# Kernel optimization log

Hardware: AMD Instinct MI355X
Metric: run time of the kernel (lower is better)

The kernel has to match this reference:

```python
import jax, jax.numpy as jnp
import numpy as np

HEAD_SIZE = 128


def setup_inputs() -> dict:
    key = jax.random.key(0)
    ks = jax.random.split(key, 6)
    B, T, C, HS, HO = 8, 2048, 1024, 128, 128
    return {
        "q": jax.random.normal(ks[0], (B, T, C), dtype=jnp.float32),
        "k": jax.random.normal(ks[1], (B, T, C), dtype=jnp.float32),
        "v": jax.random.normal(ks[2], (B, T, C), dtype=jnp.float32),
        "Wq": jax.random.normal(ks[3], (C, HS), dtype=jnp.float32) * (C ** -0.5),
        "Wk": jax.random.normal(ks[4], (C, HS), dtype=jnp.float32) * (C ** -0.5),
        "Wv": jax.random.normal(ks[5], (C, HO), dtype=jnp.float32) * (C ** -0.5),
    }


def reference(q, k, v, Wq, Wk, Wv):
    # q,k,v: [B,T,C]; Wq,Wk: [C,HS]; Wv: [C,HO]
    T = q.shape[1]
    Q = jnp.einsum("btc,ch->bth", q, Wq)  # [B,T,HS]
    K = jnp.einsum("btc,ch->bth", k, Wk)  # [B,T,HS]
    V = jnp.einsum("btc,co->bto", v, Wv)  # [B,T,HO]
    scores = jnp.einsum("bqh,bkh->bqk", Q, K)  # [B,T,T]
    # tril(ones, diagonal=1): allowed where j <= i+1; mask (set -inf) where j > i+1
    i = jnp.arange(T)[:, None]
    j = jnp.arange(T)[None, :]
    allowed = j <= i + 1  # faithful to diagonal=1 quirk
    scores = jnp.where(allowed, scores, -jnp.inf)
    weights = jax.nn.softmax(scores * (HEAD_SIZE ** -0.5), axis=-1)
    return jnp.einsum("bqk,bko->bqo", weights, V)  # [B,T,HO]
```

## Files before the change

kernel.cpp:

```cpp
#include <hip/hip_runtime.h>

typedef short short8 __attribute__((ext_vector_type(8)));
typedef float f32x4 __attribute__((ext_vector_type(4)));
typedef unsigned short ushort_t;

__device__ inline ushort_t f2bf(float f) {
    union { float f; unsigned int u; } x{f};
    unsigned int r = (x.u + 0x7fffu + ((x.u >> 16) & 1u)) >> 16;
    return (ushort_t)r;
}
__device__ inline float bf2f(ushort_t u) {
    union { unsigned int u; float f; } x{(unsigned int)u << 16};
    return x.f;
}

__device__ inline void gload_lds16(const void* g, void* l) {
    __builtin_amdgcn_global_load_lds(
        (const __attribute__((address_space(1))) unsigned int*)g,
        (__attribute__((address_space(3))) unsigned int*)l, 16, 0, 0);
}

template <int CTRL>
__device__ inline float dppadd(float x) {
    union { float f; int i; } u, v;
    u.f = x;
    v.i = __builtin_amdgcn_update_dpp(0, u.i, CTRL, 0xf, 0xf, true);
    return x + v.f;
}
#define DPP_XOR1 0xB1
#define DPP_XOR2 0x4E
#define DPP_HMIR 0x141
#define DPP_MIR  0x140

__global__ __launch_bounds__(1024) void wt_prep(const float* __restrict__ Wq,
                                                const float* __restrict__ Wk,
                                                const float* __restrict__ Wv,
                                                ushort_t* __restrict__ Wt) {
    __shared__ float t[32][33];
    int bz = blockIdx.z;
    const float* W = bz == 0 ? Wq : (bz == 1 ? Wk : Wv);
    int h0 = blockIdx.x * 32, c0 = blockIdx.y * 32;
    int tx = threadIdx.x, ty = threadIdx.y;
    t[ty][tx] = W[(c0 + ty) * 128 + h0 + tx];
    __syncthreads();
    Wt[bz * 131072 + (h0 + ty) * 1024 + c0 + tx] = f2bf(t[tx][ty]);
}

__global__ __launch_bounds__(256, 4) void proj_gemm(const float* __restrict__ q,
                                                    const float* __restrict__ k,
                                                    const float* __restrict__ v,
                                                    const ushort_t* __restrict__ Wt,
                                                    ushort_t* __restrict__ Qb,
                                                    ushort_t* __restrict__ Kb,
                                                    ushort_t* __restrict__ Vt) {
    __shared__ ushort_t lA[64][72];
    __shared__ ushort_t lB[128][72];
    int z = blockIdx.z;
    const float* X = z == 0 ? q : (z == 1 ? k : v);
    const ushort_t* Wz = Wt + z * 131072;
    int m0 = blockIdx.x * 64;
    int tid = threadIdx.x;
    int lane = tid & 63, wv = tid >> 6;
    int g = lane >> 4, li = lane & 15;

    f32x4 z4 = {0.f, 0.f, 0.f, 0.f};
    f32x4 acc[8];
#pragma unroll
    for (int n = 0; n < 8; ++n) acc[n] = z4;

    for (int ks = 0; ks < 16; ++ks) {
        int k0 = ks * 64;
        if (ks) __syncthreads();
#pragma unroll
        for (int it = 0; it < 4; ++it) {
            int idx = it * 256 + tid;
            int row = idx >> 4, c4 = idx & 15;
            const float4 val = *(const float4*)(X + (size_t)(m0 + row) * 1024 + k0 + c4 * 4);
            ushort4 bb;
            bb.x = f2bf(val.x); bb.y = f2bf(val.y); bb.z = f2bf(val.z); bb.w = f2bf(val.w);
            *(ushort4*)&lA[row][c4 * 4] = bb;
        }
#pragma unroll
        for (int it = 0; it < 4; ++it) {
            int idx = it * 256 + tid;
            int h = idx >> 3, k8 = idx & 7;
            *(int4*)&lB[h][k8 * 8] = *(const int4*)(Wz + h * 1024 + k0 + k8 * 8);
        }
        __syncthreads();
#pragma unroll
        for (int kk = 0; kk < 2; ++kk) {
            short8 a = *(const short8*)&lA[wv * 16 + li][kk * 32 + g * 8];
            short8 b[8];
#pragma unroll
            for (int n = 0; n < 8; ++n)
                b[n] = *(const short8*)&lB[n * 16 + li][kk * 32 + g * 8];
#pragma unroll
            for (int n = 0; n < 8; ++n)
                acc[n] = __builtin_amdgcn_mfma_f32_16x16x32_bf16(a, b[n], acc[n], 0, 0, 0);
        }
    }
    if (z < 2) {
        ushort_t* Out = z == 0 ? Qb : Kb;
        int rbase = m0 + wv * 16 + g * 4;
#pragma unroll
        for (int n = 0; n < 8; ++n)
#pragma unroll
            for (int r = 0; r < 4; ++r)
                Out[(size_t)(rbase + r) * 128 + n * 16 + li] = f2bf(acc[n][r]);
    } else {
        int tbase = m0 + wv * 16 + g * 4;
#pragma unroll
        for (int n = 0; n < 8; ++n)
#pragma unroll
            for (int r = 0; r < 4; ++r) {
                int t = tbase + r;
                int bb = t >> 11, tl = t & 2047;
                Vt[((size_t)bb * 128 + n * 16 + li) * 2048 + tl] = f2bf(acc[n][r]);
            }
    }
}

__global__ __launch_bounds__(256) void attn_fwd(const ushort_t* __restrict__ Qb,
                                                const ushort_t* __restrict__ Kb,
                                                const ushort_t* __restrict__ Vt,
                                                ushort_t* __restrict__ oPb,
                                                float* __restrict__ lPf) {
    constexpr float SCL = 0.08838834764831845f * 1.4426950408889634f;
    constexpr float MB  = 8.0f * 1.4426950408889634f;
    __shared__ ushort_t Kl[2][64][128];
    __shared__ ushort_t Vl[2][128][64];
    __shared__ ushort_t lP[4][16][72];

    int t = threadIdx.x;
    int lane = t & 63, wv = t >> 6;
    int g = lane >> 4, li = lane & 15;
    int b = blockIdx.x & 7;
    int idx = blockIdx.x >> 3;
    int qb = 31 - (idx >> 1);
    int s  = idx & 1;
    int r0 = qb * 64 + wv * 16;
    int NT = qb + 2; if (NT > 32) NT = 32;
    int h0 = (NT + 1) >> 1;
    int jb = s ? h0 : 0;
    int je = s ? NT : h0;
    const ushort_t* kb0 = Kb + (size_t)b * 2048 * 128;
    const ushort_t* vb0 = Vt + (size_t)b * 128 * 2048;
    ushort_t (*P)[72] = lP[wv];

    short8 qf[4];
    const ushort_t* qrow = Qb + (size_t)(b * 2048 + r0 + li) * 128 + g * 8;
#pragma unroll
    for (int kf = 0; kf < 4; ++kf) qf[kf] = *(const short8*)(qrow + kf * 32);

    f32x4 z4 = {0.f, 0.f, 0.f, 0.f};
    f32x4 o[8];
#pragma unroll
    for (int n = 0; n < 8; ++n) o[n] = z4;
    float lr[4] = {0.f, 0.f, 0.f, 0.f};

    auto STAGE = [&](int jt, int buf) {
        int j0 = jt * 64;
#pragma unroll
        for (int r = 0; r < 4; ++r) {
            int row = r * 16 + (t >> 4);
            int c = (t & 15) ^ ((t >> 4) & 7);
            gload_lds16(kb0 + (size_t)(j0 + row) * 128 + c * 8,
                        (char*)&Kl[buf][0][0] + r * 4096 + t * 16);
        }
#pragma unroll
        for (int r = 0; r < 4; ++r) {
            int row = r * 32 + (t >> 3);
            int c = (t & 7) ^ ((t >> 3) & 7);
            gload_lds16(vb0 + (size_t)row * 2048 + j0 + c * 8,
                        (char*)&Vl[buf][0][0] + r * 4096 + t * 16);
        }
    };

    STAGE(jb, 0);
    asm volatile("s_waitcnt vmcnt(0)" ::: "memory");
    __builtin_amdgcn_s_barrier();

    for (int jt = jb; jt < je; ++jt) {
        int buf = (jt - jb) & 1;
        int j0 = jt * 64;
        if (jt + 1 < je) STAGE(jt + 1, buf ^ 1);
        const char* kb = (const char*)&Kl[buf][0][0];
        const char* vb = (const char*)&Vl[buf][0][0];

        f32x4 sA[4];
#pragma unroll
        for (int jf = 0; jf < 4; ++jf) sA[jf] = z4;
#pragma unroll
        for (int jf = 0; jf < 4; ++jf)
#pragma unroll
            for (int kf = 0; kf < 4; ++kf) {
                short8 kfrag = *(const short8*)(kb + (jf * 16 + li) * 256 +
                                                (((kf * 4 + g) ^ (li & 7)) * 16));
                sA[jf] = __builtin_amdgcn_mfma_f32_16x16x32_bf16(qf[kf], kfrag, sA[jf], 0, 0, 0);
            }
        if (j0 + 63 > r0 + 1) {
#pragma unroll
            for (int jf = 0; jf < 4; ++jf)
#pragma unroll
                for (int r = 0; r < 4; ++r) {
                    int j = j0 + jf * 16 + li;
                    int i = r0 + g * 4 + r;
                    if (j > i + 1) sA[jf][r] = -1e30f;
                }
        }
#pragma unroll
        for (int jf = 0; jf < 4; ++jf)
#pragma unroll
            for (int r = 0; r < 4; ++r) {
                float p = exp2f(sA[jf][r] * SCL - MB);
                lr[r] += p;
                P[g * 4 + r][jf * 16 + li] = f2bf(p);
            }
        asm volatile("s_waitcnt lgkmcnt(0)" ::: "memory");
        __builtin_amdgcn_sched_barrier(0);
        short8 pa0 = *(const short8*)&P[li][g * 8];
        short8 pa1 = *(const short8*)&P[li][32 + g * 8];
#pragma unroll
        for (int n = 0; n < 8; ++n) {
            short8 vf = *(const short8*)(vb + (n * 16 + li) * 128 +
                                         ((g ^ (li & 7)) * 16));
            o[n] = __builtin_amdgcn_mfma_f32_16x16x32_bf16(pa0, vf, o[n], 0, 0, 0);
        }
#pragma unroll
        for (int n = 0; n < 8; ++n) {
            short8 vf = *(const short8*)(vb + (n * 16 + li) * 128 +
                                         (((4 + g) ^ (li & 7)) * 16));
            o[n] = __builtin_amdgcn_mfma_f32_16x16x32_bf16(pa1, vf, o[n], 0, 0, 0);
        }
        asm volatile("s_waitcnt vmcnt(0)" ::: "memory");
        __builtin_amdgcn_s_barrier();
    }

#pragma unroll
    for (int r = 0; r < 4; ++r) {
        lr[r] = dppadd<DPP_XOR1>(lr[r]);
        lr[r] = dppadd<DPP_XOR2>(lr[r]);
        lr[r] = dppadd<DPP_HMIR>(lr[r]);
        lr[r] = dppadd<DPP_MIR>(lr[r]);
    }
    if (li == 0) {
#pragma unroll
        for (int r = 0; r < 4; ++r)
            lPf[s * 16384 + b * 2048 + r0 + g * 4 + r] = lr[r];
    }
#pragma unroll
    for (int r = 0; r < 4; ++r) {
        size_t base = ((size_t)s * 16384 + b * 2048 + r0 + g * 4 + r) * 128 + li;
#pragma unroll
        for (int n = 0; n < 8; ++n)
            oPb[base + n * 16] = f2bf(o[n][r]);
    }
}

__global__ __launch_bounds__(256) void attn_combine(const ushort_t* __restrict__ oPb,
                                                    const float* __restrict__ lPf,
                                                    float* __restrict__ Out) {
    int gid = blockIdx.x * 256 + threadIdx.x;
    int row = gid >> 4;
    int c8 = (gid & 15) * 8;
    float inv = 1.0f / (lPf[row] + lPf[16384 + row]);
    const ushort_t* p0 = oPb + (size_t)row * 128 + c8;
    const ushort_t* p1 = p0 + (size_t)16384 * 128;
    short8 a = *(const short8*)p0;
    short8 bb = *(const short8*)p1;
    float* op = Out + (size_t)row * 128 + c8;
    float4 r0v, r1v;
    float* rp0 = (float*)&r0v;
    float* rp1 = (float*)&r1v;
#pragma unroll
    for (int j = 0; j < 4; ++j)
        rp0[j] = (bf2f((ushort_t)a[j]) + bf2f((ushort_t)bb[j])) * inv;
#pragma unroll
    for (int j = 0; j < 4; ++j)
        rp1[j] = (bf2f((ushort_t)a[4 + j]) + bf2f((ushort_t)bb[4 + j])) * inv;
    *(float4*)op = r0v;
    *(float4*)(op + 4) = r1v;
}

extern "C" void kernel_launch(void* const* d_in, const int* in_sizes, int n_in,
                              void* d_out, int out_size, void* d_ws, size_t ws_size,
                              hipStream_t stream) {
    const float* q  = (const float*)d_in[0];
    const float* k  = (const float*)d_in[1];
    const float* v  = (const float*)d_in[2];
    const float* Wq = (const float*)d_in[3];
    const float* Wk = (const float*)d_in[4];
    const float* Wv = (const float*)d_in[5];
    float* Out = (float*)d_out;

    ushort_t* Qb  = (ushort_t*)d_ws;
    ushort_t* Kb  = Qb + 2097152;
    ushort_t* Vt  = Kb + 2097152;
    ushort_t* Wt  = Vt + 2097152;
    ushort_t* oPb = Wt + 393216;
    float*    lPf = (float*)(oPb + 4194304);

    wt_prep<<<dim3(4, 32, 3), dim3(32, 32), 0, stream>>>(Wq, Wk, Wv, Wt);
    proj_gemm<<<dim3(256, 1, 3), 256, 0, stream>>>(q, k, v, Wt, Qb, Kb, Vt);
    attn_fwd<<<dim3(512), 256, 0, stream>>>(Qb, Kb, Vt, oPb, lPf);
    attn_combine<<<dim3(1024), 256, 0, stream>>>(oPb, lPf, Out);
}
```

Measured before the change: 79.26 us.

## Keep softmax probabilities in registers by transposing the QK^T MFMA

The QK^T MFMA operands are swapped so each lane holds scores for one query row across several keys. Those values can then be packed straight into the A-operand fragments of the PV MFMA. This removes the per-tile LDS write and read of P, the lgkmcnt wait and the sched barrier, and it simplifies the row-sum reduction to two cross-lane shuffles. In exchange, V fragments are now gathered with twice as many 8-byte LDS loads, permuted to match the new key ordering.

```diff
diff --git a/kernel.cpp b/kernel.cpp
--- a/kernel.cpp
+++ b/kernel.cpp
@@ -1,6 +1,7 @@
 #include <hip/hip_runtime.h>
 
 typedef short short8 __attribute__((ext_vector_type(8)));
+typedef short short4v __attribute__((ext_vector_type(4)));
 typedef float f32x4 __attribute__((ext_vector_type(4)));
 typedef unsigned short ushort_t;
 
@@ -19,18 +20,6 @@
         (const __attribute__((address_space(1))) unsigned int*)g,
         (__attribute__((address_space(3))) unsigned int*)l, 16, 0, 0);
 }
-
-template <int CTRL>
-__device__ inline float dppadd(float x) {
-    union { float f; int i; } u, v;
-    u.f = x;
-    v.i = __builtin_amdgcn_update_dpp(0, u.i, CTRL, 0xf, 0xf, true);
-    return x + v.f;
-}
-#define DPP_XOR1 0xB1
-#define DPP_XOR2 0x4E
-#define DPP_HMIR 0x141
-#define DPP_MIR  0x140
 
 __global__ __launch_bounds__(1024) void wt_prep(const float* __restrict__ Wq,
                                                 const float* __restrict__ Wk,
@@ -129,7 +118,6 @@
     constexpr float MB  = 8.0f * 1.4426950408889634f;
     __shared__ ushort_t Kl[2][64][128];
     __shared__ ushort_t Vl[2][128][64];
-    __shared__ ushort_t lP[4][16][72];
 
     int t = threadIdx.x;
     int lane = t & 63, wv = t >> 6;
@@ -145,7 +133,6 @@
     int je = s ? NT : h0;
     const ushort_t* kb0 = Kb + (size_t)b * 2048 * 128;
     const ushort_t* vb0 = Vt + (size_t)b * 128 * 2048;
-    ushort_t (*P)[72] = lP[wv];
 
     short8 qf[4];
     const ushort_t* qrow = Qb + (size_t)(b * 2048 + r0 + li) * 128 + g * 8;
@@ -156,7 +143,7 @@
     f32x4 o[8];
 #pragma unroll
     for (int n = 0; n < 8; ++n) o[n] = z4;
-    float lr[4] = {0.f, 0.f, 0.f, 0.f};
+    float lr = 0.f;
 
     auto STAGE = [&](int jt, int buf) {
         int j0 = jt * 64;
@@ -196,58 +183,54 @@
             for (int kf = 0; kf < 4; ++kf) {
                 short8 kfrag = *(const short8*)(kb + (jf * 16 + li) * 256 +
                                                 (((kf * 4 + g) ^ (li & 7)) * 16));
-                sA[jf] = __builtin_amdgcn_mfma_f32_16x16x32_bf16(qf[kf], kfrag, sA[jf], 0, 0, 0);
+                sA[jf] = __builtin_amdgcn_mfma_f32_16x16x32_bf16(kfrag, qf[kf], sA[jf], 0, 0, 0);
             }
         if (j0 + 63 > r0 + 1) {
+            int i = r0 + li;
 #pragma unroll
             for (int jf = 0; jf < 4; ++jf)
 #pragma unroll
                 for (int r = 0; r < 4; ++r) {
-                    int j = j0 + jf * 16 + li;
-                    int i = r0 + g * 4 + r;
+                    int j = j0 + jf * 16 + g * 4 + r;
                     if (j > i + 1) sA[jf][r] = -1e30f;
                 }
         }
-#pragma unroll
-        for (int jf = 0; jf < 4; ++jf)
-#pragma unroll
-            for (int r = 0; r < 4; ++r) {
-                float p = exp2f(sA[jf][r] * SCL - MB);
-                lr[r] += p;
-                P[g * 4 + r][jf * 16 + li] = f2bf(p);
-            }
-        asm volatile("s_waitcnt lgkmcnt(0)" ::: "memory");
-        __builtin_amdgcn_sched_barrier(0);
-        short8 pa0 = *(const short8*)&P[li][g * 8];
-        short8 pa1 = *(const short8*)&P[li][32 + g * 8];
+        short8 pa0, pa1;
+#pragma unroll
+        for (int r = 0; r < 4; ++r) {
+            float p0 = exp2f(sA[0][r] * SCL - MB);
+            float p1 = exp2f(sA[1][r] * SCL - MB);
+            float p2 = exp2f(sA[2][r] * SCL - MB);
+            float p3 = exp2f(sA[3][r] * SCL - MB);
+            lr += p0 + p1 + p2 + p3;
+            pa0[r]     = (short)f2bf(p0);
+            pa0[4 + r] = (short)f2bf(p1);
+            pa1[r]     = (short)f2bf(p2);
+            pa1[4 + r] = (short)f2bf(p3);
+        }
 #pragma unroll
         for (int n = 0; n < 8; ++n) {
-            short8 vf = *(const short8*)(vb + (n * 16 + li) * 128 +
-                                         ((g ^ (li & 7)) * 16));
-            o[n] = __builtin_amdgcn_mfma_f32_16x16x32_bf16(pa0, vf, o[n], 0, 0, 0);
-        }
-#pragma unroll
-        for (int n = 0; n < 8; ++n) {
-            short8 vf = *(const short8*)(vb + (n * 16 + li) * 128 +
-                                         (((4 + g) ^ (li & 7)) * 16));
-            o[n] = __builtin_amdgcn_mfma_f32_16x16x32_bf16(pa1, vf, o[n], 0, 0, 0);
+            int row = n * 16 + li;
+            const char* vrow = vb + row * 128;
+            int sw = row & 7;
+            int bo = (g & 1) * 8;
+            short4v a0 = *(const short4v*)(vrow + (((g >> 1) ^ sw) * 16) + bo);
+            short4v a1 = *(const short4v*)(vrow + (((2 + (g >> 1)) ^ sw) * 16) + bo);
+            short8 vf0 = __builtin_shufflevector(a0, a1, 0, 1, 2, 3, 4, 5, 6, 7);
+            o[n] = __builtin_amdgcn_mfma_f32_16x16x32_bf16(pa0, vf0, o[n], 0, 0, 0);
+            short4v a2 = *(const short4v*)(vrow + (((4 + (g >> 1)) ^ sw) * 16) + bo);
+            short4v a3 = *(const short4v*)(vrow + (((6 + (g >> 1)) ^ sw) * 16) + bo);
+            short8 vf1 = __builtin_shufflevector(a2, a3, 0, 1, 2, 3, 4, 5, 6, 7);
+            o[n] = __builtin_amdgcn_mfma_f32_16x16x32_bf16(pa1, vf1, o[n], 0, 0, 0);
         }
         asm volatile("s_waitcnt vmcnt(0)" ::: "memory");
         __builtin_amdgcn_s_barrier();
     }
 
-#pragma unroll
-    for (int r = 0; r < 4; ++r) {
-        lr[r] = dppadd<DPP_XOR1>(lr[r]);
-        lr[r] = dppadd<DPP_XOR2>(lr[r]);
-        lr[r] = dppadd<DPP_HMIR>(lr[r]);
-        lr[r] = dppadd<DPP_MIR>(lr[r]);
-    }
-    if (li == 0) {
-#pragma unroll
-        for (int r = 0; r < 4; ++r)
-            lPf[s * 16384 + b * 2048 + r0 + g * 4 + r] = lr[r];
-    }
+    lr += __shfl_xor(lr, 16);
+    lr += __shfl_xor(lr, 32);
+    if (g == 0)
+        lPf[s * 16384 + b * 2048 + r0 + li] = lr;
 #pragma unroll
     for (int r = 0; r < 4; ++r) {
         size_t base = ((size_t)s * 16384 + b * 2048 + r0 + g * 4 + r) * 128 + li;
```

Result: slower. 81.08 us (+2.3%).

## Switch attention to 32x32x16 MFMA with two waves of 32 rows each

Applied to the files above, without the earlier changes.

Rewrites the attention forward kernel to use 32x32x16 bf16 MFMA instead of 16x16x32. Each block now has two waves that each own 32 query rows, instead of four waves owning 16 rows each. K/V staging, the LDS swizzle, the P scratch layout and the row-sum reduction are all adapted to the new fragment layout. The goal is fewer LDS fragment reads per FLOP and denser matrix instructions. In exchange the block has fewer waves for latency hiding and each thread holds more registers.

```diff
diff --git a/kernel.cpp b/kernel.cpp
--- a/kernel.cpp
+++ b/kernel.cpp
@@ -2,6 +2,7 @@
 
 typedef short short8 __attribute__((ext_vector_type(8)));
 typedef float f32x4 __attribute__((ext_vector_type(4)));
+typedef float f32x16 __attribute__((ext_vector_type(16)));
 typedef unsigned short ushort_t;
 
 __device__ inline ushort_t f2bf(float f) {
@@ -120,7 +121,7 @@
     }
 }
 
-__global__ __launch_bounds__(256) void attn_fwd(const ushort_t* __restrict__ Qb,
+__global__ __launch_bounds__(128) void attn_fwd(const ushort_t* __restrict__ Qb,
                                                 const ushort_t* __restrict__ Kb,
                                                 const ushort_t* __restrict__ Vt,
                                                 ushort_t* __restrict__ oPb,
@@ -129,50 +130,53 @@
     constexpr float MB  = 8.0f * 1.4426950408889634f;
     __shared__ ushort_t Kl[2][64][128];
     __shared__ ushort_t Vl[2][128][64];
-    __shared__ ushort_t lP[4][16][72];
+    __shared__ ushort_t lP[2][32][76];
 
     int t = threadIdx.x;
     int lane = t & 63, wv = t >> 6;
-    int g = lane >> 4, li = lane & 15;
+    int l31 = lane & 31, h = lane >> 5;
     int b = blockIdx.x & 7;
     int idx = blockIdx.x >> 3;
     int qb = 31 - (idx >> 1);
     int s  = idx & 1;
-    int r0 = qb * 64 + wv * 16;
+    int r0 = qb * 64 + wv * 32;
     int NT = qb + 2; if (NT > 32) NT = 32;
     int h0 = (NT + 1) >> 1;
     int jb = s ? h0 : 0;
     int je = s ? NT : h0;
     const ushort_t* kb0 = Kb + (size_t)b * 2048 * 128;
     const ushort_t* vb0 = Vt + (size_t)b * 128 * 2048;
-    ushort_t (*P)[72] = lP[wv];
-
-    short8 qf[4];
-    const ushort_t* qrow = Qb + (size_t)(b * 2048 + r0 + li) * 128 + g * 8;
-#pragma unroll
-    for (int kf = 0; kf < 4; ++kf) qf[kf] = *(const short8*)(qrow + kf * 32);
-
-    f32x4 z4 = {0.f, 0.f, 0.f, 0.f};
-    f32x4 o[8];
-#pragma unroll
-    for (int n = 0; n < 8; ++n) o[n] = z4;
-    float lr[4] = {0.f, 0.f, 0.f, 0.f};
+    ushort_t (*P)[76] = lP[wv];
+
+    short8 qf[8];
+    const ushort_t* qrow = Qb + (size_t)(b * 2048 + r0 + l31) * 128 + h * 8;
+#pragma unroll
+    for (int ks = 0; ks < 8; ++ks) qf[ks] = *(const short8*)(qrow + ks * 16);
+
+    f32x16 o[4];
+#pragma unroll
+    for (int n = 0; n < 4; ++n)
+#pragma unroll
+        for (int r = 0; r < 16; ++r) o[n][r] = 0.f;
+    float lr[16];
+#pragma unroll
+    for (int r = 0; r < 16; ++r) lr[r] = 0.f;
 
     auto STAGE = [&](int jt, int buf) {
         int j0 = jt * 64;
 #pragma unroll
-        for (int r = 0; r < 4; ++r) {
-            int row = r * 16 + (t >> 4);
-            int c = (t & 15) ^ ((t >> 4) & 7);
+        for (int rr = 0; rr < 8; ++rr) {
+            int row = rr * 8 + (t >> 4);
+            int c = (t & 15) ^ ((rr & 1) * 8 + (t >> 4));
             gload_lds16(kb0 + (size_t)(j0 + row) * 128 + c * 8,
-                        (char*)&Kl[buf][0][0] + r * 4096 + t * 16);
-        }
-#pragma unroll
-        for (int r = 0; r < 4; ++r) {
-            int row = r * 32 + (t >> 3);
+                        (char*)&Kl[buf][0][0] + rr * 2048 + t * 16);
+        }
+#pragma unroll
+        for (int rr = 0; rr < 8; ++rr) {
+            int row = rr * 16 + (t >> 3);
             int c = (t & 7) ^ ((t >> 3) & 7);
             gload_lds16(vb0 + (size_t)row * 2048 + j0 + c * 8,
-                        (char*)&Vl[buf][0][0] + r * 4096 + t * 16);
+                        (char*)&Vl[buf][0][0] + rr * 2048 + t * 16);
         }
     };
 
@@ -187,74 +191,73 @@
         const char* kb = (const char*)&Kl[buf][0][0];
         const char* vb = (const char*)&Vl[buf][0][0];
 
-        f32x4 sA[4];
-#pragma unroll
-        for (int jf = 0; jf < 4; ++jf) sA[jf] = z4;
-#pragma unroll
-        for (int jf = 0; jf < 4; ++jf)
-#pragma unroll
-            for (int kf = 0; kf < 4; ++kf) {
-                short8 kfrag = *(const short8*)(kb + (jf * 16 + li) * 256 +
-                                                (((kf * 4 + g) ^ (li & 7)) * 16));
-                sA[jf] = __builtin_amdgcn_mfma_f32_16x16x32_bf16(qf[kf], kfrag, sA[jf], 0, 0, 0);
-            }
-        if (j0 + 63 > r0 + 1) {
-#pragma unroll
-            for (int jf = 0; jf < 4; ++jf)
-#pragma unroll
-                for (int r = 0; r < 4; ++r) {
-                    int j = j0 + jf * 16 + li;
-                    int i = r0 + g * 4 + r;
-                    if (j > i + 1) sA[jf][r] = -1e30f;
+#pragma unroll
+        for (int jf = 0; jf < 2; ++jf) {
+            f32x16 sf;
+#pragma unroll
+            for (int r = 0; r < 16; ++r) sf[r] = 0.f;
+            int row_t = jf * 32 + l31;
+#pragma unroll
+            for (int ks = 0; ks < 8; ++ks) {
+                int slot = (ks * 2 + h) ^ (l31 & 15);
+                short8 kfrag = *(const short8*)(kb + row_t * 256 + slot * 16);
+                sf = __builtin_amdgcn_mfma_f32_32x32x16_bf16(qf[ks], kfrag, sf, 0, 0, 0);
+            }
+            if (j0 + 63 > r0 + 1) {
+                int j = j0 + jf * 32 + l31;
+#pragma unroll
+                for (int r = 0; r < 16; ++r) {
+                    int i = r0 + (r & 3) + 8 * (r >> 2) + 4 * h;
+                    if (j > i + 1) sf[r] = -1e30f;
                 }
-        }
-#pragma unroll
-        for (int jf = 0; jf < 4; ++jf)
-#pragma unroll
-            for (int r = 0; r < 4; ++r) {
-                float p = exp2f(sA[jf][r] * SCL - MB);
+            }
+#pragma unroll
+            for (int r = 0; r < 16; ++r) {
+                float p = exp2f(sf[r] * SCL - MB);
                 lr[r] += p;
-                P[g * 4 + r][jf * 16 + li] = f2bf(p);
-            }
+                P[(r & 3) + 8 * (r >> 2) + 4 * h][jf * 32 + l31] = f2bf(p);
+            }
+        }
         asm volatile("s_waitcnt lgkmcnt(0)" ::: "memory");
         __builtin_amdgcn_sched_barrier(0);
-        short8 pa0 = *(const short8*)&P[li][g * 8];
-        short8 pa1 = *(const short8*)&P[li][32 + g * 8];
-#pragma unroll
-        for (int n = 0; n < 8; ++n) {
-            short8 vf = *(const short8*)(vb + (n * 16 + li) * 128 +
-                                         ((g ^ (li & 7)) * 16));
-            o[n] = __builtin_amdgcn_mfma_f32_16x16x32_bf16(pa0, vf, o[n], 0, 0, 0);
-        }
-#pragma unroll
-        for (int n = 0; n < 8; ++n) {
-            short8 vf = *(const short8*)(vb + (n * 16 + li) * 128 +
-                                         (((4 + g) ^ (li & 7)) * 16));
-            o[n] = __builtin_amdgcn_mfma_f32_16x16x32_bf16(pa1, vf, o[n], 0, 0, 0);
+        short8 pa[4];
+#pragma unroll
+        for (int js = 0; js < 4; ++js)
+            pa[js] = *(const short8*)((const char*)&P[0][0] + l31 * 152 + js * 32 + h * 16);
+#pragma unroll
+        for (int n = 0; n < 4; ++n) {
+            int d = n * 32 + l31;
+#pragma unroll
+            for (int js = 0; js < 4; ++js) {
+                int slot = (js * 2 + h) ^ (l31 & 7);
+                short8 vf = *(const short8*)(vb + d * 128 + slot * 16);
+                o[n] = __builtin_amdgcn_mfma_f32_32x32x16_bf16(pa[js], vf, o[n], 0, 0, 0);
+            }
         }
         asm volatile("s_waitcnt vmcnt(0)" ::: "memory");
         __builtin_amdgcn_s_barrier();
     }
 
 #pragma unroll
-    for (int r = 0; r < 4; ++r) {
+    for (int r = 0; r < 16; ++r) {
         lr[r] = dppadd<DPP_XOR1>(lr[r]);
         lr[r] = dppadd<DPP_XOR2>(lr[r]);
         lr[r] = dppadd<DPP_HMIR>(lr[r]);
         lr[r] = dppadd<DPP_MIR>(lr[r]);
-    }
-    if (li == 0) {
-#pragma unroll
-        for (int r = 0; r < 4; ++r)
-            lPf[s * 16384 + b * 2048 + r0 + g * 4 + r] = lr[r];
-    }
-#pragma unroll
-    for (int r = 0; r < 4; ++r) {
-        size_t base = ((size_t)s * 16384 + b * 2048 + r0 + g * 4 + r) * 128 + li;
-#pragma unroll
-        for (int n = 0; n < 8; ++n)
-            oPb[base + n * 16] = f2bf(o[n][r]);
-    }
+        lr[r] += __shfl_xor(lr[r], 16);
+    }
+    if (l31 == 0) {
+#pragma unroll
+        for (int r = 0; r < 16; ++r)
+            lPf[s * 16384 + b * 2048 + r0 + (r & 3) + 8 * (r >> 2) + 4 * h] = lr[r];
+    }
+#pragma unroll
+    for (int n = 0; n < 4; ++n)
+#pragma unroll
+        for (int r = 0; r < 16; ++r) {
+            int qq = r0 + (r & 3) + 8 * (r >> 2) + 4 * h;
+            oPb[((size_t)s * 16384 + b * 2048 + qq) * 128 + n * 32 + l31] = f2bf(o[n][r]);
+        }
 }
 
 __global__ __launch_bounds__(256) void attn_combine(const ushort_t* __restrict__ oPb,
@@ -302,6 +305,6 @@
 
     wt_prep<<<dim3(4, 32, 3), dim3(32, 32), 0, stream>>>(Wq, Wk, Wv, Wt);
     proj_gemm<<<dim3(256, 1, 3), 256, 0, stream>>>(q, k, v, Wt, Qb, Kb, Vt);
-    attn_fwd<<<dim3(512), 256, 0, stream>>>(Qb, Kb, Vt, oPb, lPf);
+    attn_fwd<<<dim3(512), 128, 0, stream>>>(Qb, Kb, Vt, oPb, lPf);
     attn_combine<<<dim3(1024), 256, 0, stream>>>(oPb, lPf, Out);
 }
```

After: 94.48 us. 19.2% more time.
